# Performance work log

Measured on AMD Instinct MI355X. Metric: run time of the kernel, lower is better.

The kernel has to match this reference:

```python
import jax, jax.numpy as jnp
import numpy as np
import math

D_MODEL = 512
N_HEADS = 8
PATH_LEN = 3
B, L, S = 4, 1024, 1024


def _path_index_structure(L, S, path_length):
    """Precompute the static multi-hop index structure (numpy, trace-time)."""
    i = np.arange(L)[:, None]          # [L,1]
    j = np.arange(S)[None, :]          # [1,S]
    step = (j - i) / path_length       # float
    # Python int() truncates toward zero; i + k*step >= 0 here, so floor == int().
    m1 = np.floor(i + 1 * step).astype(np.int32)  # [L,S] first intermediate point
    m2 = np.floor(i + 2 * step).astype(np.int32)  # [L,S] second intermediate point
    near = np.abs(i - j) <= path_length            # [L,S] bool: direct-score region
    return m1, m2, near


def setup_inputs() -> dict:
    key = jax.random.key(0)
    ks = jax.random.split(key, 7)
    inp = {
        "queries": jax.random.normal(ks[0], (B, L, D_MODEL), dtype=jnp.float32),
        "keys": jax.random.normal(ks[1], (B, S, D_MODEL), dtype=jnp.float32),
        "values": jax.random.normal(ks[2], (B, S, D_MODEL), dtype=jnp.float32),
        # nn.Linear(d_model, d_keys*n_heads, bias=False): stored as [in, out] so y = x @ W
        "W_q": jax.random.normal(ks[3], (D_MODEL, D_MODEL), dtype=jnp.float32) * 0.02,
        "W_k": jax.random.normal(ks[4], (D_MODEL, D_MODEL), dtype=jnp.float32) * 0.02,
        "W_v": jax.random.normal(ks[5], (D_MODEL, D_MODEL), dtype=jnp.float32) * 0.02,
        "W_o": jax.random.normal(ks[6], (D_MODEL, D_MODEL), dtype=jnp.float32) * 0.02,
    }
    return inp


def reference(queries, keys, values, W_q, W_k, W_v, W_o):
    Bv, Lv, _ = queries.shape
    Sv = keys.shape[1]
    H = N_HEADS
    q = (queries @ W_q).reshape(Bv, Lv, H, -1).transpose(0, 2, 1, 3)  # [B,H,L,D]
    k = (keys @ W_k).reshape(Bv, Sv, H, -1).transpose(0, 2, 1, 3)     # [B,H,S,D]
    v = (values @ W_v).reshape(Bv, Sv, H, -1).transpose(0, 2, 1, 3)   # [B,H,S,D]
    D = q.shape[-1]

    scores = jnp.einsum('bhld,bhsd->bhls', q, k) / math.sqrt(D)  # [B,H,L,S]

    # --- path-score modification (vectorized form of the nested loops) ---
    m1, m2, near = _path_index_structure(Lv, Sv, PATH_LEN)
    row = np.arange(Lv)[:, None]
    col = np.arange(Sv)[None, :]
    a = scores[:, :, row, m1]   # scores[:,:,i,m1(i,j)] -> [B,H,L,S]
    b = scores[:, :, m2, col]   # scores[:,:,m2(i,j),j] -> [B,H,L,S]
    # .mean() in the original reduces over BOTH batch and heads to a scalar per (i,j)
    path_mean = jnp.mean(a * b, axis=(0, 1))  # [L,S]
    scores = jnp.where(jnp.asarray(near), scores, path_mean[None, None, :, :])

    attn = jax.nn.softmax(scores, axis=-1)  # dropout p=0 in eval reference
    out = jnp.einsum('bhls,bhsd->blhd', attn, v).reshape(Bv, Lv, H * D)
    out = out @ W_o  # [B,L,d_model]
    return out, attn
```

## Files before the change

kernel.cpp:

```cpp
#include <hip/hip_runtime.h>
#include <math.h>

static constexpr int B_ = 4;
static constexpr int L_ = 1024;
static constexpr int S_ = 1024;
static constexpr int DMODEL = 512;
static constexpr int NH = 8;
static constexpr int DH = 64;
static constexpr int NBH = 32;

typedef __attribute__((ext_vector_type(8))) short s8;
typedef __attribute__((ext_vector_type(4))) float floatx4;

__device__ __forceinline__ short f2bf(float f) {
  unsigned u = __float_as_uint(f);
  return (short)((u + 0x7fffu + ((u >> 16) & 1u)) >> 16);
}
__device__ __forceinline__ float bf2f(short s) {
  return __uint_as_float(((unsigned)(unsigned short)s) << 16);
}

__global__ __launch_bounds__(256)
void cvt_inputs_kernel(const float* __restrict__ q, const float* __restrict__ k,
                       const float* __restrict__ v, short* __restrict__ dst) {
  const int i = blockIdx.x * 256 + threadIdx.x;
  const int arr = i >> 18;
  const int off = (i & 262143) << 3;
  const float* src = (arr == 0) ? q : (arr == 1) ? k : v;
  const float4 f0 = *(const float4*)(src + off);
  const float4 f1 = *(const float4*)(src + off + 4);
  s8 o;
  o[0] = f2bf(f0.x); o[1] = f2bf(f0.y); o[2] = f2bf(f0.z); o[3] = f2bf(f0.w);
  o[4] = f2bf(f1.x); o[5] = f2bf(f1.y); o[6] = f2bf(f1.z); o[7] = f2bf(f1.w);
  *(s8*)(dst + (size_t)arr * 2097152 + off) = o;
}

__global__ __launch_bounds__(256)
void wtrans_kernel(const float* __restrict__ Wq, const float* __restrict__ Wk,
                   const float* __restrict__ Wv, const float* __restrict__ Wo,
                   short* __restrict__ WT) {
  __shared__ float t[32][33];
  const int z = blockIdx.z;
  const float* W = (z == 0) ? Wq : (z == 1) ? Wk : (z == 2) ? Wv : Wo;
  short* dst = WT + (size_t)z * 262144;
  const int k0 = blockIdx.y * 32, n0 = blockIdx.x * 32;
  const int row = threadIdx.x >> 3;
  const int c4 = (threadIdx.x & 7) << 2;
  const float4 f = *(const float4*)(W + (size_t)(k0 + row) * 512 + n0 + c4);
  t[row][c4 + 0] = f.x; t[row][c4 + 1] = f.y; t[row][c4 + 2] = f.z; t[row][c4 + 3] = f.w;
  __syncthreads();
#pragma unroll
  for (int j = 0; j < 4; ++j)
    dst[(size_t)(n0 + row) * 512 + k0 + c4 + j] = f2bf(t[c4 + j][row]);
}

template<int MODE>
__global__ __launch_bounds__(256)
void proj_mfma_kernel(const short* __restrict__ A, const short* __restrict__ WT,
                      void* __restrict__ C, short* __restrict__ C2, int K) {
  const int tid = threadIdx.x;
  const int lane = tid & 63, w = tid >> 6;
  const int wm = w >> 1, wn = w & 1;
  const int m0 = blockIdx.y * 64, n0 = blockIdx.x * 64;
  const int kl = (lane >> 4) << 3;
  const int rA = m0 + wm * 32 + (lane & 15);
  const int rB = n0 + wn * 32 + (lane & 15);
  const short* pA = A + (size_t)rA * K + kl;
  const short* pB = WT + (size_t)rB * K + kl;
  const size_t f16K = (size_t)16 * K;
  floatx4 acc00 = {0,0,0,0}, acc01 = {0,0,0,0}, acc10 = {0,0,0,0}, acc11 = {0,0,0,0};
  for (int k = 0; k < K; k += 32) {
    const s8 a0 = *(const s8*)(pA + k);
    const s8 a1 = *(const s8*)(pA + f16K + k);
    const s8 b0 = *(const s8*)(pB + k);
    const s8 b1 = *(const s8*)(pB + f16K + k);
    acc00 = __builtin_amdgcn_mfma_f32_16x16x32_bf16(a0, b0, acc00, 0, 0, 0);
    acc01 = __builtin_amdgcn_mfma_f32_16x16x32_bf16(a0, b1, acc01, 0, 0, 0);
    acc10 = __builtin_amdgcn_mfma_f32_16x16x32_bf16(a1, b0, acc10, 0, 0, 0);
    acc11 = __builtin_amdgcn_mfma_f32_16x16x32_bf16(a1, b1, acc11, 0, 0, 0);
  }
  const int crow = (lane >> 4) << 2;
  const int ccol = lane & 15;
#pragma unroll
  for (int fm = 0; fm < 2; ++fm)
#pragma unroll
    for (int fn = 0; fn < 2; ++fn) {
      const floatx4 acc = (fm == 0) ? ((fn == 0) ? acc00 : acc01)
                                    : ((fn == 0) ? acc10 : acc11);
      const int col = n0 + wn * 32 + fn * 16 + ccol;
#pragma unroll
      for (int r = 0; r < 4; ++r) {
        const int row = m0 + wm * 32 + fm * 16 + crow + r;
        if (MODE == 0) {
          const int b = row >> 10, l = row & 1023, h = col >> 6, d = col & 63;
          ((short*)C)[((size_t)((b * NH + h) * L_ + l)) * DH + d] = f2bf(acc[r]);
        } else if (MODE == 3) {
          const int b = row >> 10, s = row & 1023, h = col >> 6, d = col & 63;
          const short val = f2bf(acc[r]);
          ((short*)C)[((size_t)((b * NH + h) * DH + d)) * S_ + s] = val;
          C2[((size_t)((b * NH + h) * S_ + s)) * DH + d] = val;
        } else {
          ((float*)C)[(size_t)row * DMODEL + col] = acc[r];
        }
      }
    }
}

__global__ __launch_bounds__(256)
void scores_mfma_kernel(const short* __restrict__ qbf, const short* __restrict__ kbf,
                        float* __restrict__ Sc) {
  const int tid = threadIdx.x;
  const int lane = tid & 63, w = tid >> 6;
  const int wm = w >> 1, wn = w & 1;
  const int m0 = blockIdx.y * 64, n0 = blockIdx.x * 64;
  const int bh = blockIdx.z;
  const int kl = (lane >> 4) << 3;
  const short* pA = qbf + (size_t)bh * L_ * DH + (size_t)(m0 + wm * 32 + (lane & 15)) * DH + kl;
  const short* pB = kbf + (size_t)bh * S_ * DH + (size_t)(n0 + wn * 32 + (lane & 15)) * DH + kl;
  floatx4 acc00 = {0,0,0,0}, acc01 = {0,0,0,0}, acc10 = {0,0,0,0}, acc11 = {0,0,0,0};
#pragma unroll
  for (int k = 0; k < DH; k += 32) {
    const s8 a0 = *(const s8*)(pA + k);
    const s8 a1 = *(const s8*)(pA + 16 * DH + k);
    const s8 b0 = *(const s8*)(pB + k);
    const s8 b1 = *(const s8*)(pB + 16 * DH + k);
    acc00 = __builtin_amdgcn_mfma_f32_16x16x32_bf16(a0, b0, acc00, 0, 0, 0);
    acc01 = __builtin_amdgcn_mfma_f32_16x16x32_bf16(a0, b1, acc01, 0, 0, 0);
    acc10 = __builtin_amdgcn_mfma_f32_16x16x32_bf16(a1, b0, acc10, 0, 0, 0);
    acc11 = __builtin_amdgcn_mfma_f32_16x16x32_bf16(a1, b1, acc11, 0, 0, 0);
  }
  float* Cp = Sc + (size_t)bh * L_ * S_;
  const int crow = (lane >> 4) << 2;
  const int ccol = lane & 15;
#pragma unroll
  for (int fm = 0; fm < 2; ++fm)
#pragma unroll
    for (int fn = 0; fn < 2; ++fn) {
      const floatx4 acc = (fm == 0) ? ((fn == 0) ? acc00 : acc01)
                                    : ((fn == 0) ? acc10 : acc11);
      const int col = n0 + wn * 32 + fn * 16 + ccol;
#pragma unroll
      for (int r = 0; r < 4; ++r) {
        const int row = m0 + wm * 32 + fm * 16 + crow + r;
        Cp[(size_t)row * S_ + col] = acc[r] * 0.125f;
      }
    }
}

__global__ __launch_bounds__(256)
void path_mean_kernel(const float* __restrict__ Sc, float* __restrict__ pm) {
  __shared__ float As[32][36];
  __shared__ float Bs[32][36];
  const int orig = blockIdx.x;
  const int wgid = (orig & 7) * 128 + (orig >> 3);
  const int i0 = (wgid >> 5) << 5;
  const int j0 = (wgid & 31) << 5;
  const int c0 = (2 * i0 + j0) / 3;
  const int c0_al = c0 & ~3;
  const int r0 = (i0 + 2 * j0) / 3;
  const int tid = threadIdx.x;
  const int row_s = tid >> 3;
  const int c4 = tid & 7;
  const int ti = tid >> 3;
  const int tj = tid & 7;
  const int gi = i0 + ti;
  int aoff[4], boff[4];
#pragma unroll
  for (int b = 0; b < 4; ++b) {
    const int gj = j0 + 4 * tj + b;
    const int m1 = (2 * gi + gj) / 3;
    const int m2 = (gi + 2 * gj) / 3;
    aoff[b] = ti * 36 + (m1 - c0_al);
    boff[b] = (m2 - r0) * 36 + (4 * tj + b);
  }
  const int gcA = c0_al + 4 * c4;
  int gcA2 = c0_al + 32; if (gcA2 > 1020) gcA2 = 1020;
  const float* pA  = Sc + (size_t)(i0 + row_s) * S_ + gcA;
  const float* pA2 = Sc + (size_t)(i0 + (tid & 31)) * S_ + gcA2;
  const float* pB  = Sc + (size_t)(r0 + row_s) * S_ + j0 + 4 * c4;
  const float* As0 = &As[0][0];
  const float* Bs0 = &Bs[0][0];
  float acc[4] = {0.f, 0.f, 0.f, 0.f};
  for (int z = 0; z < NBH; ++z) {
    const size_t zo = (size_t)z * (L_ * S_);
    const float4 av = *(const float4*)(pA + zo);
    const float4 bv = *(const float4*)(pB + zo);
    float4 av2;
    if (tid < 32) av2 = *(const float4*)(pA2 + zo);
    __syncthreads();
    *(float4*)&As[row_s][4 * c4] = av;
    if (tid < 32) *(float4*)&As[tid][32] = av2;
    *(float4*)&Bs[row_s][4 * c4] = bv;
    __syncthreads();
#pragma unroll
    for (int b = 0; b < 4; ++b)
      acc[b] = fmaf(As0[aoff[b]], Bs0[boff[b]], acc[b]);
  }
  float4 o = make_float4(acc[0] * (1.f / 32.f), acc[1] * (1.f / 32.f),
                         acc[2] * (1.f / 32.f), acc[3] * (1.f / 32.f));
  *(float4*)&pm[(size_t)gi * S_ + j0 + 4 * tj] = o;
}

__global__ __launch_bounds__(256)
void pm_stats_kernel(const float* __restrict__ pm, short* __restrict__ E,
                     float* __restrict__ pmmax, float* __restrict__ pmsum) {
  const int wid = threadIdx.x >> 6, lane = threadIdx.x & 63;
  const int i = blockIdx.x * 4 + wid;
  const float* row = pm + (size_t)i * S_;
  const int j0 = lane << 4;
  float v[16];
#pragma unroll
  for (int c = 0; c < 4; ++c) {
    const float4 f = *(const float4*)(row + j0 + c * 4);
    v[c * 4 + 0] = f.x; v[c * 4 + 1] = f.y; v[c * 4 + 2] = f.z; v[c * 4 + 3] = f.w;
  }
  float mx = -1e30f;
#pragma unroll
  for (int u = 0; u < 16; ++u) {
    const int d = i - (j0 + u);
    const bool far = (d > 3) || (d < -3);
    if (far) mx = fmaxf(mx, v[u]);
  }
#pragma unroll
  for (int off = 32; off >= 1; off >>= 1) mx = fmaxf(mx, __shfl_xor(mx, off));
  float sum = 0.f;
  short e[16];
#pragma unroll
  for (int u = 0; u < 16; ++u) {
    const int d = i - (j0 + u);
    const bool far = (d > 3) || (d < -3);
    const float ev = far ? __expf(v[u] - mx) : 0.f;
    sum += ev;
    e[u] = f2bf(ev);
  }
#pragma unroll
  for (int off = 32; off >= 1; off >>= 1) sum += __shfl_xor(sum, off);
  s8 o0, o1;
#pragma unroll
  for (int u = 0; u < 8; ++u) { o0[u] = e[u]; o1[u] = e[8 + u]; }
  short* Erow = E + (size_t)i * S_ + j0;
  *(s8*)Erow = o0;
  *(s8*)(Erow + 8) = o1;
  if (lane == 0) { pmmax[i] = mx; pmsum[i] = sum; }
}

__global__ __launch_bounds__(256)
void attn_write_kernel(float* __restrict__ Sc, const short* __restrict__ E,
                       const float* __restrict__ pmmax, const float* __restrict__ pmsum,
                       float* __restrict__ cvec, float* __restrict__ band) {
  const int wid = threadIdx.x >> 6, lane = threadIdx.x & 63;
  const int i = blockIdx.x * 4 + wid;
  const int bh = blockIdx.y;
  float* row = Sc + ((size_t)bh * L_ + i) * S_;

  const int j_u = i - 3 + lane;
  float s_u = -1e30f;
  if (lane < 7 && j_u >= 0 && j_u < S_) s_u = row[j_u];

  float bm = s_u;
#pragma unroll
  for (int off = 32; off >= 1; off >>= 1) bm = fmaxf(bm, __shfl_xor(bm, off));
  const float pmx = pmmax[i];
  const float m = fmaxf(pmx, bm);
  const float bexp = __expf(s_u - m);
  float bsum = bexp;
#pragma unroll
  for (int off = 32; off >= 1; off >>= 1) bsum += __shfl_xor(bsum, off);
  const float cpm = __expf(pmx - m);
  const float inv = 1.f / (bsum + pmsum[i] * cpm);
  const float c = cpm * inv;

  if (lane == 0) cvec[bh * L_ + i] = c;
  if (lane < 8) band[((size_t)(bh * L_ + i)) << 3 | lane] = __expf(s_u - m) * inv;

  const short* Erow = E + (size_t)i * S_;
  const int j0 = lane << 4;
  const s8 e0 = *(const s8*)(Erow + j0);
  const s8 e1 = *(const s8*)(Erow + j0 + 8);
  float outv[16];
#pragma unroll
  for (int u = 0; u < 8; ++u) {
    outv[u]     = bf2f(e0[u]) * c;
    outv[8 + u] = bf2f(e1[u]) * c;
  }
#pragma unroll
  for (int t = 0; t < 16; ++t) {
    const int j = j0 + t;
    const int d = j - i;
    if (d >= -3 && d <= 3)
      outv[t] = __expf(row[j] - m) * inv;
  }
#pragma unroll
  for (int c4 = 0; c4 < 4; ++c4)
    *(float4*)(row + j0 + c4 * 4) =
        make_float4(outv[c4 * 4], outv[c4 * 4 + 1], outv[c4 * 4 + 2], outv[c4 * 4 + 3]);
}

__global__ __launch_bounds__(256)
void ev_kernel(const short* __restrict__ E, const short* __restrict__ vT,
               const short* __restrict__ vS, const float* __restrict__ cvec,
               const float* __restrict__ band, short* __restrict__ out1) {
  const int tid = threadIdx.x;
  const int lane = tid & 63, w = tid >> 6;
  const int wm = w >> 1, wn = w & 1;
  const int m0 = blockIdx.x * 64;
  const int bh = blockIdx.y;
  const int b = bh >> 3, h = bh & 7;
  const int kl = (lane >> 4) << 3;
  const short* pA = E + (size_t)(m0 + wm * 32 + (lane & 15)) * S_ + kl;
  const short* pB = vT + (size_t)bh * DH * S_ + (size_t)(wn * 32 + (lane & 15)) * S_ + kl;
  floatx4 acc00 = {0,0,0,0}, acc01 = {0,0,0,0}, acc10 = {0,0,0,0}, acc11 = {0,0,0,0};
  for (int k = 0; k < S_; k += 32) {
    const s8 a0 = *(const s8*)(pA + k);
    const s8 a1 = *(const s8*)(pA + 16 * S_ + k);
    const s8 b0 = *(const s8*)(pB + k);
    const s8 b1 = *(const s8*)(pB + 16 * S_ + k);
    acc00 = __builtin_amdgcn_mfma_f32_16x16x32_bf16(a0, b0, acc00, 0, 0, 0);
    acc01 = __builtin_amdgcn_mfma_f32_16x16x32_bf16(a0, b1, acc01, 0, 0, 0);
    acc10 = __builtin_amdgcn_mfma_f32_16x16x32_bf16(a1, b0, acc10, 0, 0, 0);
    acc11 = __builtin_amdgcn_mfma_f32_16x16x32_bf16(a1, b1, acc11, 0, 0, 0);
  }
  const int crow = (lane >> 4) << 2;
  const int ccol = lane & 15;
#pragma unroll
  for (int fm = 0; fm < 2; ++fm)
#pragma unroll
    for (int r = 0; r < 4; ++r) {
      const int l = m0 + wm * 32 + fm * 16 + crow + r;
      const float c = cvec[bh * L_ + l];
      const float* bap = band + (((size_t)(bh * L_ + l)) << 3);
      const float4 b0v = *(const float4*)bap;
      const float4 b1v = *(const float4*)(bap + 4);
      const float bav[7] = {b0v.x, b0v.y, b0v.z, b0v.w, b1v.x, b1v.y, b1v.z};
#pragma unroll
      for (int fn = 0; fn < 2; ++fn) {
        const floatx4 acc = (fm == 0) ? ((fn == 0) ? acc00 : acc01)
                                      : ((fn == 0) ? acc10 : acc11);
        const int d = wn * 32 + fn * 16 + ccol;
        float corr = 0.f;
#pragma unroll
        for (int u = 0; u < 7; ++u) {
          int j = l - 3 + u;
          const int jc = j < 0 ? 0 : (j > 1023 ? 1023 : j);
          corr = fmaf(bav[u], bf2f(vS[((size_t)bh * S_ + jc) * DH + d]), corr);
        }
        const float val = fmaf(c, acc[r], corr);
        out1[((size_t)(b * L_ + l)) * DMODEL + h * DH + d] = f2bf(val);
      }
    }
}

extern "C" void kernel_launch(void* const* d_in, const int* in_sizes, int n_in,
                              void* d_out, int out_size, void* d_ws, size_t ws_size,
                              hipStream_t stream) {
  const float* queries = (const float*)d_in[0];
  const float* keys    = (const float*)d_in[1];
  const float* values  = (const float*)d_in[2];
  const float* Wq      = (const float*)d_in[3];
  const float* Wk      = (const float*)d_in[4];
  const float* Wv      = (const float*)d_in[5];
  const float* Wo      = (const float*)d_in[6];

  float* out  = (float*)d_out;
  float* attn = out + (size_t)B_ * L_ * DMODEL;

  char* ws = (char*)d_ws;
  short* xbf  = (short*)(ws);
  short* WT   = (short*)(ws + 12u * 1048576);
  short* qbf  = (short*)(ws + 14u * 1048576);
  short* kbf  = (short*)(ws + 18u * 1048576);
  short* vT   = (short*)(ws + 22u * 1048576);
  short* vS   = (short*)(ws + 26u * 1048576);
  float* pm   = (float*)(ws + 30u * 1048576);
  short* E    = (short*)(ws + 34u * 1048576);
  float* pmmax= (float*)(ws + 36u * 1048576);
  float* pmsum= (float*)(ws + 36u * 1048576 + 4096);
  float* cvec = (float*)(ws + 36u * 1048576 + 65536);
  float* band = (float*)(ws + 37u * 1048576);
  short* out1 = (short*)(ws + 38u * 1048576);

  const dim3 blk(256);

  hipLaunchKernelGGL(cvt_inputs_kernel, dim3(3072), blk, 0, stream,
                     queries, keys, values, xbf);
  hipLaunchKernelGGL(wtrans_kernel, dim3(16, 16, 4), blk, 0, stream,
                     Wq, Wk, Wv, Wo, WT);

  const dim3 gProj(DMODEL / 64, (B_ * L_) / 64);
  hipLaunchKernelGGL((proj_mfma_kernel<0>), gProj, blk, 0, stream,
                     xbf,           WT,          (void*)qbf, (short*)nullptr, DMODEL);
  hipLaunchKernelGGL((proj_mfma_kernel<0>), gProj, blk, 0, stream,
                     xbf + 2097152, WT + 262144, (void*)kbf, (short*)nullptr, DMODEL);
  hipLaunchKernelGGL((proj_mfma_kernel<3>), gProj, blk, 0, stream,
                     xbf + 4194304, WT + 524288, (void*)vT,  vS,              DMODEL);

  const dim3 gSc(S_ / 64, L_ / 64, NBH);
  hipLaunchKernelGGL(scores_mfma_kernel, gSc, blk, 0, stream, qbf, kbf, attn);

  hipLaunchKernelGGL(path_mean_kernel, dim3(1024), blk, 0, stream, attn, pm);

  hipLaunchKernelGGL(pm_stats_kernel, dim3(L_ / 4), blk, 0, stream,
                     pm, E, pmmax, pmsum);

  hipLaunchKernelGGL(attn_write_kernel, dim3(L_ / 4, NBH), blk, 0, stream,
                     attn, E, pmmax, pmsum, cvec, band);

  hipLaunchKernelGGL(ev_kernel, dim3(L_ / 64, NBH), blk, 0, stream,
                     E, vT, vS, cvec, band, out1);

  hipLaunchKernelGGL((proj_mfma_kernel<2>), gProj, blk, 0, stream,
                     out1, WT + 786432, (void*)out, (short*)nullptr, DMODEL);
}
```

Measured before the change: 225.6 us.

## Fuse score computation into path-mean kernel and stop materializing full scores

The separate scores GEMM that wrote the full fp32 [B,H,L,S] score tensor is removed. The path-mean kernel now recomputes the needed 32x32 QK^T tiles per (b,h) with MFMA into LDS and reduces across waves. The attn-write kernel recomputes only the 7 near-diagonal scores as short dot products. In addition, the Q and K projections are batched into one launch over a z-dimension, and ev_kernel stages its band of V rows in LDS. Together these remove a large round trip of the score tensor through global memory, at the cost of redundant MFMA work (two tiles per block per bh) and a serial per-wave loop over heads.

Result: no change. 227.1 us (+0.7%).

```diff
diff --git a/kernel.cpp b/kernel.cpp
--- a/kernel.cpp
+++ b/kernel.cpp
@@ -58,6 +58,9 @@
 __global__ __launch_bounds__(256)
 void proj_mfma_kernel(const short* __restrict__ A, const short* __restrict__ WT,
                       void* __restrict__ C, short* __restrict__ C2, int K) {
+  const int z = blockIdx.z;
+  A  += (size_t)z * 2097152;
+  WT += (size_t)z * 262144;
   const int tid = threadIdx.x;
   const int lane = tid & 63, w = tid >> 6;
   const int wm = w >> 1, wn = w & 1;
@@ -93,7 +96,8 @@
         const int row = m0 + wm * 32 + fm * 16 + crow + r;
         if (MODE == 0) {
           const int b = row >> 10, l = row & 1023, h = col >> 6, d = col & 63;
-          ((short*)C)[((size_t)((b * NH + h) * L_ + l)) * DH + d] = f2bf(acc[r]);
+          ((short*)C)[(size_t)z * 2097152 +
+                      ((size_t)((b * NH + h) * L_ + l)) * DH + d] = f2bf(acc[r]);
         } else if (MODE == 3) {
           const int b = row >> 10, s = row & 1023, h = col >> 6, d = col & 63;
           const short val = f2bf(acc[r]);
@@ -107,98 +111,101 @@
 }
 
 __global__ __launch_bounds__(256)
-void scores_mfma_kernel(const short* __restrict__ qbf, const short* __restrict__ kbf,
-                        float* __restrict__ Sc) {
-  const int tid = threadIdx.x;
-  const int lane = tid & 63, w = tid >> 6;
-  const int wm = w >> 1, wn = w & 1;
-  const int m0 = blockIdx.y * 64, n0 = blockIdx.x * 64;
-  const int bh = blockIdx.z;
-  const int kl = (lane >> 4) << 3;
-  const short* pA = qbf + (size_t)bh * L_ * DH + (size_t)(m0 + wm * 32 + (lane & 15)) * DH + kl;
-  const short* pB = kbf + (size_t)bh * S_ * DH + (size_t)(n0 + wn * 32 + (lane & 15)) * DH + kl;
-  floatx4 acc00 = {0,0,0,0}, acc01 = {0,0,0,0}, acc10 = {0,0,0,0}, acc11 = {0,0,0,0};
-#pragma unroll
-  for (int k = 0; k < DH; k += 32) {
-    const s8 a0 = *(const s8*)(pA + k);
-    const s8 a1 = *(const s8*)(pA + 16 * DH + k);
-    const s8 b0 = *(const s8*)(pB + k);
-    const s8 b1 = *(const s8*)(pB + 16 * DH + k);
-    acc00 = __builtin_amdgcn_mfma_f32_16x16x32_bf16(a0, b0, acc00, 0, 0, 0);
-    acc01 = __builtin_amdgcn_mfma_f32_16x16x32_bf16(a0, b1, acc01, 0, 0, 0);
-    acc10 = __builtin_amdgcn_mfma_f32_16x16x32_bf16(a1, b0, acc10, 0, 0, 0);
-    acc11 = __builtin_amdgcn_mfma_f32_16x16x32_bf16(a1, b1, acc11, 0, 0, 0);
-  }
-  float* Cp = Sc + (size_t)bh * L_ * S_;
-  const int crow = (lane >> 4) << 2;
-  const int ccol = lane & 15;
-#pragma unroll
-  for (int fm = 0; fm < 2; ++fm)
-#pragma unroll
-    for (int fn = 0; fn < 2; ++fn) {
-      const floatx4 acc = (fm == 0) ? ((fn == 0) ? acc00 : acc01)
-                                    : ((fn == 0) ? acc10 : acc11);
-      const int col = n0 + wn * 32 + fn * 16 + ccol;
-#pragma unroll
-      for (int r = 0; r < 4; ++r) {
-        const int row = m0 + wm * 32 + fm * 16 + crow + r;
-        Cp[(size_t)row * S_ + col] = acc[r] * 0.125f;
-      }
-    }
-}
-
-__global__ __launch_bounds__(256)
-void path_mean_kernel(const float* __restrict__ Sc, float* __restrict__ pm) {
-  __shared__ float As[32][36];
-  __shared__ float Bs[32][36];
+void pm_fused_kernel(const short* __restrict__ qbf, const short* __restrict__ kbf,
+                     float* __restrict__ pm) {
+  __shared__ __align__(16) float SA[4][32][33];
+  __shared__ __align__(16) float SB[4][32][33];
+
   const int orig = blockIdx.x;
   const int wgid = (orig & 7) * 128 + (orig >> 3);
   const int i0 = (wgid >> 5) << 5;
   const int j0 = (wgid & 31) << 5;
   const int c0 = (2 * i0 + j0) / 3;
-  const int c0_al = c0 & ~3;
   const int r0 = (i0 + 2 * j0) / 3;
+
   const int tid = threadIdx.x;
-  const int row_s = tid >> 3;
-  const int c4 = tid & 7;
-  const int ti = tid >> 3;
-  const int tj = tid & 7;
-  const int gi = i0 + ti;
-  int aoff[4], boff[4];
-#pragma unroll
-  for (int b = 0; b < 4; ++b) {
-    const int gj = j0 + 4 * tj + b;
+  const int lane = tid & 63, w = tid >> 6;
+  const int frow = lane & 15;
+  const int kl = (lane >> 4) << 3;
+  const int ti = lane & 31;
+  const int tjb = (lane >> 5) << 4;
+
+  int aoff[16], boff[16];
+#pragma unroll
+  for (int u = 0; u < 16; ++u) {
+    const int gi = i0 + ti, gj = j0 + tjb + u;
     const int m1 = (2 * gi + gj) / 3;
     const int m2 = (gi + 2 * gj) / 3;
-    aoff[b] = ti * 36 + (m1 - c0_al);
-    boff[b] = (m2 - r0) * 36 + (4 * tj + b);
-  }
-  const int gcA = c0_al + 4 * c4;
-  int gcA2 = c0_al + 32; if (gcA2 > 1020) gcA2 = 1020;
-  const float* pA  = Sc + (size_t)(i0 + row_s) * S_ + gcA;
-  const float* pA2 = Sc + (size_t)(i0 + (tid & 31)) * S_ + gcA2;
-  const float* pB  = Sc + (size_t)(r0 + row_s) * S_ + j0 + 4 * c4;
-  const float* As0 = &As[0][0];
-  const float* Bs0 = &Bs[0][0];
-  float acc[4] = {0.f, 0.f, 0.f, 0.f};
-  for (int z = 0; z < NBH; ++z) {
-    const size_t zo = (size_t)z * (L_ * S_);
-    const float4 av = *(const float4*)(pA + zo);
-    const float4 bv = *(const float4*)(pB + zo);
-    float4 av2;
-    if (tid < 32) av2 = *(const float4*)(pA2 + zo);
-    __syncthreads();
-    *(float4*)&As[row_s][4 * c4] = av;
-    if (tid < 32) *(float4*)&As[tid][32] = av2;
-    *(float4*)&Bs[row_s][4 * c4] = bv;
-    __syncthreads();
-#pragma unroll
-    for (int b = 0; b < 4; ++b)
-      acc[b] = fmaf(As0[aoff[b]], Bs0[boff[b]], acc[b]);
-  }
-  float4 o = make_float4(acc[0] * (1.f / 32.f), acc[1] * (1.f / 32.f),
-                         acc[2] * (1.f / 32.f), acc[3] * (1.f / 32.f));
-  *(float4*)&pm[(size_t)gi * S_ + j0 + 4 * tj] = o;
+    aoff[u] = ti * 33 + (m1 - c0);
+    boff[u] = (m2 - r0) * 33 + (tjb + u);
+  }
+  float acc[16];
+#pragma unroll
+  for (int u = 0; u < 16; ++u) acc[u] = 0.f;
+
+  float* SAw = &SA[w][0][0];
+  float* SBw = &SB[w][0][0];
+  const int crow = (lane >> 4) << 2;
+  const int ccol = lane & 15;
+
+  for (int bh = w; bh < NBH; bh += 4) {
+    const short* Qb = qbf + (size_t)bh * L_ * DH;
+    const short* Kb = kbf + (size_t)bh * S_ * DH;
+#pragma unroll
+    for (int t = 0; t < 2; ++t) {
+      const int rb = t ? r0 : i0;
+      const int cb = t ? j0 : c0;
+      const short* pQ = Qb + (size_t)(rb + frow) * DH + kl;
+      const short* pK = Kb + (size_t)(cb + frow) * DH + kl;
+      floatx4 a00 = {0,0,0,0}, a01 = {0,0,0,0}, a10 = {0,0,0,0}, a11 = {0,0,0,0};
+#pragma unroll
+      for (int ks = 0; ks < DH; ks += 32) {
+        const s8 qa = *(const s8*)(pQ + ks);
+        const s8 qb2 = *(const s8*)(pQ + 16 * DH + ks);
+        const s8 ka = *(const s8*)(pK + ks);
+        const s8 kb2 = *(const s8*)(pK + 16 * DH + ks);
+        a00 = __builtin_amdgcn_mfma_f32_16x16x32_bf16(qa,  ka,  a00, 0, 0, 0);
+        a01 = __builtin_amdgcn_mfma_f32_16x16x32_bf16(qa,  kb2, a01, 0, 0, 0);
+        a10 = __builtin_amdgcn_mfma_f32_16x16x32_bf16(qb2, ka,  a10, 0, 0, 0);
+        a11 = __builtin_amdgcn_mfma_f32_16x16x32_bf16(qb2, kb2, a11, 0, 0, 0);
+      }
+      float* dst = t ? SBw : SAw;
+#pragma unroll
+      for (int fm = 0; fm < 2; ++fm)
+#pragma unroll
+        for (int fn = 0; fn < 2; ++fn) {
+          const floatx4 a = (fm == 0) ? ((fn == 0) ? a00 : a01)
+                                      : ((fn == 0) ? a10 : a11);
+#pragma unroll
+          for (int r = 0; r < 4; ++r)
+            dst[(fm * 16 + crow + r) * 33 + fn * 16 + ccol] = a[r] * 0.125f;
+        }
+    }
+#pragma unroll
+    for (int u = 0; u < 16; ++u)
+      acc[u] = fmaf(SAw[aoff[u]], SBw[boff[u]], acc[u]);
+  }
+
+  __syncthreads();
+  float* P = &SA[0][0][0];
+#pragma unroll
+  for (int u4 = 0; u4 < 4; ++u4) {
+    float4 v4 = make_float4(acc[u4 * 4], acc[u4 * 4 + 1],
+                            acc[u4 * 4 + 2], acc[u4 * 4 + 3]);
+    *(float4*)&P[w * 1152 + ti * 36 + tjb + u4 * 4] = v4;
+  }
+  __syncthreads();
+  const int ti2 = tid >> 3;
+  const int tj2 = (tid & 7) << 2;
+  float4 ssum = make_float4(0.f, 0.f, 0.f, 0.f);
+#pragma unroll
+  for (int w2 = 0; w2 < 4; ++w2) {
+    const float4 v = *(const float4*)&P[w2 * 1152 + ti2 * 36 + tj2];
+    ssum.x += v.x; ssum.y += v.y; ssum.z += v.z; ssum.w += v.w;
+  }
+  ssum.x *= (1.f / 32.f); ssum.y *= (1.f / 32.f);
+  ssum.z *= (1.f / 32.f); ssum.w *= (1.f / 32.f);
+  *(float4*)&pm[(size_t)(i0 + ti2) * S_ + j0 + tj2] = ssum;
 }
 
 __global__ __launch_bounds__(256)
@@ -245,17 +252,29 @@
 }
 
 __global__ __launch_bounds__(256)
-void attn_write_kernel(float* __restrict__ Sc, const short* __restrict__ E,
+void attn_write_kernel(float* __restrict__ attnOut, const short* __restrict__ E,
                        const float* __restrict__ pmmax, const float* __restrict__ pmsum,
+                       const short* __restrict__ qbf, const short* __restrict__ kbf,
                        float* __restrict__ cvec, float* __restrict__ band) {
   const int wid = threadIdx.x >> 6, lane = threadIdx.x & 63;
   const int i = blockIdx.x * 4 + wid;
   const int bh = blockIdx.y;
-  float* row = Sc + ((size_t)bh * L_ + i) * S_;
 
   const int j_u = i - 3 + lane;
   float s_u = -1e30f;
-  if (lane < 7 && j_u >= 0 && j_u < S_) s_u = row[j_u];
+  if (lane < 7 && j_u >= 0 && j_u < S_) {
+    const short* qr = qbf + ((size_t)bh * L_ + i) * DH;
+    const short* kr = kbf + ((size_t)bh * S_ + j_u) * DH;
+    float d0 = 0.f;
+#pragma unroll
+    for (int c = 0; c < 8; ++c) {
+      const s8 qv = *(const s8*)(qr + c * 8);
+      const s8 kv = *(const s8*)(kr + c * 8);
+#pragma unroll
+      for (int e = 0; e < 8; ++e) d0 = fmaf(bf2f(qv[e]), bf2f(kv[e]), d0);
+    }
+    s_u = d0 * 0.125f;
+  }
 
   float bm = s_u;
 #pragma unroll
@@ -271,8 +290,13 @@
   const float c = cpm * inv;
 
   if (lane == 0) cvec[bh * L_ + i] = c;
-  if (lane < 8) band[((size_t)(bh * L_ + i)) << 3 | lane] = __expf(s_u - m) * inv;
-
+  if (lane < 8) band[((size_t)(bh * L_ + i)) << 3 | lane] = bexp * inv;
+
+  float bb[7];
+#pragma unroll
+  for (int u = 0; u < 7; ++u) bb[u] = __shfl(bexp, u) * inv;
+
+  float* row = attnOut + ((size_t)bh * L_ + i) * S_;
   const short* Erow = E + (size_t)i * S_;
   const int j0 = lane << 4;
   const s8 e0 = *(const s8*)(Erow + j0);
@@ -285,10 +309,8 @@
   }
 #pragma unroll
   for (int t = 0; t < 16; ++t) {
-    const int j = j0 + t;
-    const int d = j - i;
-    if (d >= -3 && d <= 3)
-      outv[t] = __expf(row[j] - m) * inv;
+    const int d = (j0 + t) - i;
+    if (d >= -3 && d <= 3) outv[t] = bb[d + 3];
   }
 #pragma unroll
   for (int c4 = 0; c4 < 4; ++c4)
@@ -300,12 +322,21 @@
 void ev_kernel(const short* __restrict__ E, const short* __restrict__ vT,
                const short* __restrict__ vS, const float* __restrict__ cvec,
                const float* __restrict__ band, short* __restrict__ out1) {
+  __shared__ short Vb[70 * 64];
   const int tid = threadIdx.x;
-  const int lane = tid & 63, w = tid >> 6;
-  const int wm = w >> 1, wn = w & 1;
   const int m0 = blockIdx.x * 64;
   const int bh = blockIdx.y;
   const int b = bh >> 3, h = bh & 7;
+
+  for (int idx = tid; idx < 560; idx += 256) {
+    const int rr = idx >> 3, c8 = (idx & 7) << 3;
+    int j = m0 - 3 + rr; j = j < 0 ? 0 : (j > 1023 ? 1023 : j);
+    *(s8*)&Vb[rr * 64 + c8] = *(const s8*)(vS + ((size_t)bh * S_ + j) * DH + c8);
+  }
+  __syncthreads();
+
+  const int lane = tid & 63, w = tid >> 6;
+  const int wm = w >> 1, wn = w & 1;
   const int kl = (lane >> 4) << 3;
   const short* pA = E + (size_t)(m0 + wm * 32 + (lane & 15)) * S_ + kl;
   const short* pB = vT + (size_t)bh * DH * S_ + (size_t)(wn * 32 + (lane & 15)) * S_ + kl;
@@ -327,6 +358,7 @@
 #pragma unroll
     for (int r = 0; r < 4; ++r) {
       const int l = m0 + wm * 32 + fm * 16 + crow + r;
+      const int lrel = (l - m0);
       const float c = cvec[bh * L_ + l];
       const float* bap = band + (((size_t)(bh * L_ + l)) << 3);
       const float4 b0v = *(const float4*)bap;
@@ -339,11 +371,8 @@
         const int d = wn * 32 + fn * 16 + ccol;
         float corr = 0.f;
 #pragma unroll
-        for (int u = 0; u < 7; ++u) {
-          int j = l - 3 + u;
-          const int jc = j < 0 ? 0 : (j > 1023 ? 1023 : j);
-          corr = fmaf(bav[u], bf2f(vS[((size_t)bh * S_ + jc) * DH + d]), corr);
-        }
+        for (int u = 0; u < 7; ++u)
+          corr = fmaf(bav[u], bf2f(Vb[(lrel + u) * 64 + d]), corr);
         const float val = fmaf(c, acc[r], corr);
         out1[((size_t)(b * L_ + l)) * DMODEL + h * DH + d] = f2bf(val);
       }
@@ -386,24 +415,20 @@
   hipLaunchKernelGGL(wtrans_kernel, dim3(16, 16, 4), blk, 0, stream,
                      Wq, Wk, Wv, Wo, WT);
 
+  const dim3 gProjQK(DMODEL / 64, (B_ * L_) / 64, 2);
+  hipLaunchKernelGGL((proj_mfma_kernel<0>), gProjQK, blk, 0, stream,
+                     xbf, WT, (void*)qbf, (short*)nullptr, DMODEL);
   const dim3 gProj(DMODEL / 64, (B_ * L_) / 64);
-  hipLaunchKernelGGL((proj_mfma_kernel<0>), gProj, blk, 0, stream,
-                     xbf,           WT,          (void*)qbf, (short*)nullptr, DMODEL);
-  hipLaunchKernelGGL((proj_mfma_kernel<0>), gProj, blk, 0, stream,
-                     xbf + 2097152, WT + 262144, (void*)kbf, (short*)nullptr, DMODEL);
   hipLaunchKernelGGL((proj_mfma_kernel<3>), gProj, blk, 0, stream,
-                     xbf + 4194304, WT + 524288, (void*)vT,  vS,              DMODEL);
-
-  const dim3 gSc(S_ / 64, L_ / 64, NBH);
-  hipLaunchKernelGGL(scores_mfma_kernel, gSc, blk, 0, stream, qbf, kbf, attn);
-
-  hipLaunchKernelGGL(path_mean_kernel, dim3(1024), blk, 0, stream, attn, pm);
+                     xbf + 4194304, WT + 524288, (void*)vT, vS, DMODEL);
+
+  hipLaunchKernelGGL(pm_fused_kernel, dim3(1024), blk, 0, stream, qbf, kbf, pm);
 
   hipLaunchKernelGGL(pm_stats_kernel, dim3(L_ / 4), blk, 0, stream,
                      pm, E, pmmax, pmsum);
 
   hipLaunchKernelGGL(attn_write_kernel, dim3(L_ / 4, NBH), blk, 0, stream,
-                     attn, E, pmmax, pmsum, cvec, band);
+                     attn, E, pmmax, pmsum, qbf, kbf, cvec, band);
 
   hipLaunchKernelGGL(ev_kernel, dim3(L_ / 64, NBH), blk, 0, stream,
                      E, vT, vS, cvec, band, out1);
```

## Store scores in bf16 scratch, fuse attn write into EV kernel, merge QKV projections

Applied to the files above, without the earlier changes.

Scores are written as bf16 to a workspace buffer instead of fp32 into the attn output, with the diagonal band saved separately in fp32. The path-mean kernel reads the bf16 scores, and the separate attn_write pass is folded into the E·V MFMA loop, which writes final attention rows while streaming E. The three QKV projections become one launch, and V band rows are staged in shared memory. The goal is to cut the fp32 score write/read traffic and launch count; path_mean now uses bf16-rounded scores, which lowers its precision.

After: 202.2 us (median of 2 runs). 10.4% less time.

```diff
diff --git a/kernel.cpp b/kernel.cpp
--- a/kernel.cpp
+++ b/kernel.cpp
@@ -22,8 +22,14 @@
 
 __global__ __launch_bounds__(256)
 void cvt_inputs_kernel(const float* __restrict__ q, const float* __restrict__ k,
-                       const float* __restrict__ v, short* __restrict__ dst) {
+                       const float* __restrict__ v, short* __restrict__ dst,
+                       float* __restrict__ bandS) {
   const int i = blockIdx.x * 256 + threadIdx.x;
+  if (i < 32768) {
+    const float4 m4 = make_float4(-1e30f, -1e30f, -1e30f, -1e30f);
+    *(float4*)(bandS + ((size_t)i << 3)) = m4;
+    *(float4*)(bandS + ((size_t)i << 3) + 4) = m4;
+  }
   const int arr = i >> 18;
   const int off = (i & 262143) << 3;
   const float* src = (arr == 0) ? q : (arr == 1) ? k : v;
@@ -54,19 +60,21 @@
     dst[(size_t)(n0 + row) * 512 + k0 + c4 + j] = f2bf(t[c4 + j][row]);
 }
 
-template<int MODE>
-__global__ __launch_bounds__(256)
-void proj_mfma_kernel(const short* __restrict__ A, const short* __restrict__ WT,
-                      void* __restrict__ C, short* __restrict__ C2, int K) {
+__global__ __launch_bounds__(256)
+void proj_qkv_kernel(const short* __restrict__ xbf, const short* __restrict__ WTall,
+                     short* __restrict__ qk, short* __restrict__ vT,
+                     short* __restrict__ vS) {
+  const int z = blockIdx.z;
+  const short* A = xbf + (size_t)z * 2097152;
+  const short* WT = WTall + (size_t)z * 262144;
+  const int K = DMODEL;
   const int tid = threadIdx.x;
   const int lane = tid & 63, w = tid >> 6;
   const int wm = w >> 1, wn = w & 1;
   const int m0 = blockIdx.y * 64, n0 = blockIdx.x * 64;
   const int kl = (lane >> 4) << 3;
-  const int rA = m0 + wm * 32 + (lane & 15);
-  const int rB = n0 + wn * 32 + (lane & 15);
-  const short* pA = A + (size_t)rA * K + kl;
-  const short* pB = WT + (size_t)rB * K + kl;
+  const short* pA = A + (size_t)(m0 + wm * 32 + (lane & 15)) * K + kl;
+  const short* pB = WT + (size_t)(n0 + wn * 32 + (lane & 15)) * K + kl;
   const size_t f16K = (size_t)16 * K;
   floatx4 acc00 = {0,0,0,0}, acc01 = {0,0,0,0}, acc10 = {0,0,0,0}, acc11 = {0,0,0,0};
   for (int k = 0; k < K; k += 32) {
@@ -91,24 +99,21 @@
 #pragma unroll
       for (int r = 0; r < 4; ++r) {
         const int row = m0 + wm * 32 + fm * 16 + crow + r;
-        if (MODE == 0) {
-          const int b = row >> 10, l = row & 1023, h = col >> 6, d = col & 63;
-          ((short*)C)[((size_t)((b * NH + h) * L_ + l)) * DH + d] = f2bf(acc[r]);
-        } else if (MODE == 3) {
-          const int b = row >> 10, s = row & 1023, h = col >> 6, d = col & 63;
-          const short val = f2bf(acc[r]);
-          ((short*)C)[((size_t)((b * NH + h) * DH + d)) * S_ + s] = val;
-          C2[((size_t)((b * NH + h) * S_ + s)) * DH + d] = val;
+        const int b = row >> 10, l = row & 1023, h = col >> 6, d = col & 63;
+        const short val = f2bf(acc[r]);
+        if (z < 2) {
+          qk[(size_t)z * 2097152 + ((size_t)((b * NH + h) * L_ + l)) * DH + d] = val;
         } else {
-          ((float*)C)[(size_t)row * DMODEL + col] = acc[r];
+          vT[((size_t)((b * NH + h) * DH + d)) * S_ + l] = val;
+          vS[((size_t)((b * NH + h) * S_ + l)) * DH + d] = val;
         }
       }
     }
 }
 
 __global__ __launch_bounds__(256)
-void scores_mfma_kernel(const short* __restrict__ qbf, const short* __restrict__ kbf,
-                        float* __restrict__ Sc) {
+void scores_bf16_kernel(const short* __restrict__ qbf, const short* __restrict__ kbf,
+                        short* __restrict__ Sbf, float* __restrict__ bandS) {
   const int tid = threadIdx.x;
   const int lane = tid & 63, w = tid >> 6;
   const int wm = w >> 1, wn = w & 1;
@@ -129,7 +134,7 @@
     acc10 = __builtin_amdgcn_mfma_f32_16x16x32_bf16(a1, b0, acc10, 0, 0, 0);
     acc11 = __builtin_amdgcn_mfma_f32_16x16x32_bf16(a1, b1, acc11, 0, 0, 0);
   }
-  float* Cp = Sc + (size_t)bh * L_ * S_;
+  short* Sp = Sbf + ((size_t)bh << 20);
   const int crow = (lane >> 4) << 2;
   const int ccol = lane & 15;
 #pragma unroll
@@ -142,25 +147,27 @@
 #pragma unroll
       for (int r = 0; r < 4; ++r) {
         const int row = m0 + wm * 32 + fm * 16 + crow + r;
-        Cp[(size_t)row * S_ + col] = acc[r] * 0.125f;
-      }
-    }
-}
-
-__global__ __launch_bounds__(256)
-void path_mean_kernel(const float* __restrict__ Sc, float* __restrict__ pm) {
-  __shared__ float As[32][36];
+        const float sc = acc[r] * 0.125f;
+        Sp[(size_t)row * S_ + col] = f2bf(sc);
+        const int dd = col - row;
+        if (dd >= -3 && dd <= 3)
+          bandS[(((size_t)bh << 10) + row) * 8 + dd + 3] = sc;
+      }
+    }
+}
+
+__global__ __launch_bounds__(256)
+void path_mean_kernel(const short* __restrict__ Sbf, float* __restrict__ pm) {
+  __shared__ float As[32][44];
   __shared__ float Bs[32][36];
   const int orig = blockIdx.x;
   const int wgid = (orig & 7) * 128 + (orig >> 3);
   const int i0 = (wgid >> 5) << 5;
   const int j0 = (wgid & 31) << 5;
   const int c0 = (2 * i0 + j0) / 3;
-  const int c0_al = c0 & ~3;
+  const int c0a = c0 & ~7;
   const int r0 = (i0 + 2 * j0) / 3;
   const int tid = threadIdx.x;
-  const int row_s = tid >> 3;
-  const int c4 = tid & 7;
   const int ti = tid >> 3;
   const int tj = tid & 7;
   const int gi = i0 + ti;
@@ -170,27 +177,50 @@
     const int gj = j0 + 4 * tj + b;
     const int m1 = (2 * gi + gj) / 3;
     const int m2 = (gi + 2 * gj) / 3;
-    aoff[b] = ti * 36 + (m1 - c0_al);
+    aoff[b] = ti * 44 + (m1 - c0a);
     boff[b] = (m2 - r0) * 36 + (4 * tj + b);
   }
-  const int gcA = c0_al + 4 * c4;
-  int gcA2 = c0_al + 32; if (gcA2 > 1020) gcA2 = 1020;
-  const float* pA  = Sc + (size_t)(i0 + row_s) * S_ + gcA;
-  const float* pA2 = Sc + (size_t)(i0 + (tid & 31)) * S_ + gcA2;
-  const float* pB  = Sc + (size_t)(r0 + row_s) * S_ + j0 + 4 * c4;
+  const int uA = tid;
+  const int uB2 = tid + 256;
+  int arow = 0, ac = 0, brow = 0, bc = 0, brow2 = 0, bc2 = 0;
+  bool isA = uA < 160;
+  if (isA) { arow = uA / 5; ac = uA - arow * 5; }
+  else { const int v = uA - 160; brow = v >> 2; bc = v & 3; }
+  const bool hasU2 = tid < 32;
+  { const int v = uB2 - 160; brow2 = v >> 2; bc2 = v & 3; }
+  int gcA = c0a + (ac << 3); if (gcA > 1016) gcA = 1016;
+  const short* pA = Sbf + (size_t)(i0 + arow) * S_ + gcA;
+  const short* pB = Sbf + (size_t)(r0 + brow) * S_ + j0 + (bc << 3);
+  const short* pB2 = Sbf + (size_t)(r0 + brow2) * S_ + j0 + (bc2 << 3);
+
   const float* As0 = &As[0][0];
   const float* Bs0 = &Bs[0][0];
   float acc[4] = {0.f, 0.f, 0.f, 0.f};
   for (int z = 0; z < NBH; ++z) {
-    const size_t zo = (size_t)z * (L_ * S_);
-    const float4 av = *(const float4*)(pA + zo);
-    const float4 bv = *(const float4*)(pB + zo);
-    float4 av2;
-    if (tid < 32) av2 = *(const float4*)(pA2 + zo);
+    const size_t zo = (size_t)z << 20;
+    const s8 v1 = isA ? *(const s8*)(pA + zo) : *(const s8*)(pB + zo);
+    s8 v2;
+    if (hasU2) v2 = *(const s8*)(pB2 + zo);
     __syncthreads();
-    *(float4*)&As[row_s][4 * c4] = av;
-    if (tid < 32) *(float4*)&As[tid][32] = av2;
-    *(float4*)&Bs[row_s][4 * c4] = bv;
+    {
+      float4 lo, hi;
+      lo.x = bf2f(v1[0]); lo.y = bf2f(v1[1]); lo.z = bf2f(v1[2]); lo.w = bf2f(v1[3]);
+      hi.x = bf2f(v1[4]); hi.y = bf2f(v1[5]); hi.z = bf2f(v1[6]); hi.w = bf2f(v1[7]);
+      if (isA) {
+        *(float4*)&As[arow][ac << 3] = lo;
+        *(float4*)&As[arow][(ac << 3) + 4] = hi;
+      } else {
+        *(float4*)&Bs[brow][bc << 3] = lo;
+        *(float4*)&Bs[brow][(bc << 3) + 4] = hi;
+      }
+      if (hasU2) {
+        float4 lo2, hi2;
+        lo2.x = bf2f(v2[0]); lo2.y = bf2f(v2[1]); lo2.z = bf2f(v2[2]); lo2.w = bf2f(v2[3]);
+        hi2.x = bf2f(v2[4]); hi2.y = bf2f(v2[5]); hi2.z = bf2f(v2[6]); hi2.w = bf2f(v2[7]);
+        *(float4*)&Bs[brow2][bc2 << 3] = lo2;
+        *(float4*)&Bs[brow2][(bc2 << 3) + 4] = hi2;
+      }
+    }
     __syncthreads();
 #pragma unroll
     for (int b = 0; b < 4; ++b)
@@ -245,70 +275,59 @@
 }
 
 __global__ __launch_bounds__(256)
-void attn_write_kernel(float* __restrict__ Sc, const short* __restrict__ E,
-                       const float* __restrict__ pmmax, const float* __restrict__ pmsum,
-                       float* __restrict__ cvec, float* __restrict__ band) {
-  const int wid = threadIdx.x >> 6, lane = threadIdx.x & 63;
-  const int i = blockIdx.x * 4 + wid;
-  const int bh = blockIdx.y;
-  float* row = Sc + ((size_t)bh * L_ + i) * S_;
-
-  const int j_u = i - 3 + lane;
-  float s_u = -1e30f;
-  if (lane < 7 && j_u >= 0 && j_u < S_) s_u = row[j_u];
-
-  float bm = s_u;
-#pragma unroll
-  for (int off = 32; off >= 1; off >>= 1) bm = fmaxf(bm, __shfl_xor(bm, off));
-  const float pmx = pmmax[i];
-  const float m = fmaxf(pmx, bm);
-  const float bexp = __expf(s_u - m);
-  float bsum = bexp;
-#pragma unroll
-  for (int off = 32; off >= 1; off >>= 1) bsum += __shfl_xor(bsum, off);
-  const float cpm = __expf(pmx - m);
-  const float inv = 1.f / (bsum + pmsum[i] * cpm);
-  const float c = cpm * inv;
-
-  if (lane == 0) cvec[bh * L_ + i] = c;
-  if (lane < 8) band[((size_t)(bh * L_ + i)) << 3 | lane] = __expf(s_u - m) * inv;
-
-  const short* Erow = E + (size_t)i * S_;
-  const int j0 = lane << 4;
-  const s8 e0 = *(const s8*)(Erow + j0);
-  const s8 e1 = *(const s8*)(Erow + j0 + 8);
-  float outv[16];
-#pragma unroll
-  for (int u = 0; u < 8; ++u) {
-    outv[u]     = bf2f(e0[u]) * c;
-    outv[8 + u] = bf2f(e1[u]) * c;
-  }
-#pragma unroll
-  for (int t = 0; t < 16; ++t) {
-    const int j = j0 + t;
-    const int d = j - i;
-    if (d >= -3 && d <= 3)
-      outv[t] = __expf(row[j] - m) * inv;
-  }
-#pragma unroll
-  for (int c4 = 0; c4 < 4; ++c4)
-    *(float4*)(row + j0 + c4 * 4) =
-        make_float4(outv[c4 * 4], outv[c4 * 4 + 1], outv[c4 * 4 + 2], outv[c4 * 4 + 3]);
-}
-
-__global__ __launch_bounds__(256)
-void ev_kernel(const short* __restrict__ E, const short* __restrict__ vT,
-               const short* __restrict__ vS, const float* __restrict__ cvec,
-               const float* __restrict__ band, short* __restrict__ out1) {
+void ev_fused_kernel(const short* __restrict__ E, const short* __restrict__ vT,
+                     const short* __restrict__ vS, const float* __restrict__ bandS,
+                     const float* __restrict__ pmmax, const float* __restrict__ pmsum,
+                     float* __restrict__ attn, short* __restrict__ out1) {
+  __shared__ float cL[64];
+  __shared__ float bL[64][8];
+  __shared__ short Vb[70 * 64];
   const int tid = threadIdx.x;
-  const int lane = tid & 63, w = tid >> 6;
-  const int wm = w >> 1, wn = w & 1;
   const int m0 = blockIdx.x * 64;
   const int bh = blockIdx.y;
   const int b = bh >> 3, h = bh & 7;
+
+  for (int idx = tid; idx < 560; idx += 256) {
+    const int rr = idx >> 3, c8 = (idx & 7) << 3;
+    int j = m0 - 3 + rr; j = j < 0 ? 0 : (j > 1023 ? 1023 : j);
+    *(s8*)&Vb[rr * 64 + c8] = *(const s8*)(vS + ((size_t)bh * S_ + j) * DH + c8);
+  }
+
+  {
+    const int r = tid >> 2, p = tid & 3;
+    const int l = m0 + r;
+    const float pmx = pmmax[l], psum = pmsum[l];
+    const float* bs = bandS + (((size_t)bh << 10) + l) * 8;
+    const float sa = bs[p], sb2 = bs[p + 4];
+    float mx = fmaxf(sa, sb2);
+    mx = fmaxf(mx, __shfl_xor(mx, 1));
+    mx = fmaxf(mx, __shfl_xor(mx, 2));
+    const float m = fmaxf(mx, pmx);
+    const float ea = __expf(sa - m), eb = __expf(sb2 - m);
+    float bsum = ea + eb;
+    bsum += __shfl_xor(bsum, 1);
+    bsum += __shfl_xor(bsum, 2);
+    const float cpm = __expf(pmx - m);
+    const float inv = 1.f / (bsum + psum * cpm);
+    if (p == 0) cL[r] = cpm * inv;
+    bL[r][p] = ea * inv;
+    bL[r][p + 4] = eb * inv;
+  }
+  __syncthreads();
+
+  const int lane = tid & 63, w = tid >> 6;
+  const int wm = w >> 1, wn = w & 1;
+  const int frow = lane & 15;
   const int kl = (lane >> 4) << 3;
-  const short* pA = E + (size_t)(m0 + wm * 32 + (lane & 15)) * S_ + kl;
-  const short* pB = vT + (size_t)bh * DH * S_ + (size_t)(wn * 32 + (lane & 15)) * S_ + kl;
+  const int ra0 = m0 + wm * 32 + frow;
+  const int lr0 = wm * 32 + frow;
+  const int lr1 = lr0 + 16;
+  const short* pA = E + (size_t)ra0 * S_ + kl;
+  const short* pB = vT + (size_t)bh * DH * S_ + (size_t)(wn * 32 + frow) * S_ + kl;
+  const float c0v = cL[lr0];
+  const float c1v = cL[lr1];
+  float* arow0 = attn + ((size_t)bh * L_ + ra0) * S_;
+  float* arow1 = arow0 + (size_t)16 * S_;
   floatx4 acc00 = {0,0,0,0}, acc01 = {0,0,0,0}, acc10 = {0,0,0,0}, acc11 = {0,0,0,0};
   for (int k = 0; k < S_; k += 32) {
     const s8 a0 = *(const s8*)(pA + k);
@@ -319,18 +338,49 @@
     acc01 = __builtin_amdgcn_mfma_f32_16x16x32_bf16(a0, b1, acc01, 0, 0, 0);
     acc10 = __builtin_amdgcn_mfma_f32_16x16x32_bf16(a1, b0, acc10, 0, 0, 0);
     acc11 = __builtin_amdgcn_mfma_f32_16x16x32_bf16(a1, b1, acc11, 0, 0, 0);
-  }
+    const int jw = k + kl;
+    if (wn == 0) {
+      float att[8];
+#pragma unroll
+      for (int e = 0; e < 8; ++e) att[e] = bf2f(a0[e]) * c0v;
+      const int rel = ra0 - jw;
+      if ((unsigned)(rel + 3) <= 13u) {
+#pragma unroll
+        for (int e = 0; e < 8; ++e) {
+          const int d = e - rel;
+          if ((unsigned)(d + 3) <= 6u) att[e] = bL[lr0][d + 3];
+        }
+      }
+      *(float4*)(arow0 + jw) = make_float4(att[0], att[1], att[2], att[3]);
+      *(float4*)(arow0 + jw + 4) = make_float4(att[4], att[5], att[6], att[7]);
+    } else {
+      float att[8];
+#pragma unroll
+      for (int e = 0; e < 8; ++e) att[e] = bf2f(a1[e]) * c1v;
+      const int rel = ra0 + 16 - jw;
+      if ((unsigned)(rel + 3) <= 13u) {
+#pragma unroll
+        for (int e = 0; e < 8; ++e) {
+          const int d = e - rel;
+          if ((unsigned)(d + 3) <= 6u) att[e] = bL[lr1][d + 3];
+        }
+      }
+      *(float4*)(arow1 + jw) = make_float4(att[0], att[1], att[2], att[3]);
+      *(float4*)(arow1 + jw + 4) = make_float4(att[4], att[5], att[6], att[7]);
+    }
+  }
+
   const int crow = (lane >> 4) << 2;
   const int ccol = lane & 15;
 #pragma unroll
   for (int fm = 0; fm < 2; ++fm)
 #pragma unroll
     for (int r = 0; r < 4; ++r) {
-      const int l = m0 + wm * 32 + fm * 16 + crow + r;
-      const float c = cvec[bh * L_ + l];
-      const float* bap = band + (((size_t)(bh * L_ + l)) << 3);
-      const float4 b0v = *(const float4*)bap;
-      const float4 b1v = *(const float4*)(bap + 4);
+      const int lrel = wm * 32 + fm * 16 + crow + r;
+      const int l = m0 + lrel;
+      const float cc = cL[lrel];
+      const float4 b0v = *(const float4*)&bL[lrel][0];
+      const float4 b1v = *(const float4*)&bL[lrel][4];
       const float bav[7] = {b0v.x, b0v.y, b0v.z, b0v.w, b1v.x, b1v.y, b1v.z};
 #pragma unroll
       for (int fn = 0; fn < 2; ++fn) {
@@ -339,13 +389,50 @@
         const int d = wn * 32 + fn * 16 + ccol;
         float corr = 0.f;
 #pragma unroll
-        for (int u = 0; u < 7; ++u) {
-          int j = l - 3 + u;
-          const int jc = j < 0 ? 0 : (j > 1023 ? 1023 : j);
-          corr = fmaf(bav[u], bf2f(vS[((size_t)bh * S_ + jc) * DH + d]), corr);
-        }
-        const float val = fmaf(c, acc[r], corr);
+        for (int u = 0; u < 7; ++u)
+          corr = fmaf(bav[u], bf2f(Vb[(lrel + u) * 64 + d]), corr);
+        const float val = fmaf(cc, acc[r], corr);
         out1[((size_t)(b * L_ + l)) * DMODEL + h * DH + d] = f2bf(val);
+      }
+    }
+}
+
+__global__ __launch_bounds__(256)
+void proj_out_kernel(const short* __restrict__ A, const short* __restrict__ WT,
+                     float* __restrict__ C) {
+  const int K = DMODEL;
+  const int tid = threadIdx.x;
+  const int lane = tid & 63, w = tid >> 6;
+  const int wm = w >> 1, wn = w & 1;
+  const int m0 = blockIdx.y * 64, n0 = blockIdx.x * 64;
+  const int kl = (lane >> 4) << 3;
+  const short* pA = A + (size_t)(m0 + wm * 32 + (lane & 15)) * K + kl;
+  const short* pB = WT + (size_t)(n0 + wn * 32 + (lane & 15)) * K + kl;
+  const size_t f16K = (size_t)16 * K;
+  floatx4 acc00 = {0,0,0,0}, acc01 = {0,0,0,0}, acc10 = {0,0,0,0}, acc11 = {0,0,0,0};
+  for (int k = 0; k < K; k += 32) {
+    const s8 a0 = *(const s8*)(pA + k);
+    const s8 a1 = *(const s8*)(pA + f16K + k);
+    const s8 b0 = *(const s8*)(pB + k);
+    const s8 b1 = *(const s8*)(pB + f16K + k);
+    acc00 = __builtin_amdgcn_mfma_f32_16x16x32_bf16(a0, b0, acc00, 0, 0, 0);
+    acc01 = __builtin_amdgcn_mfma_f32_16x16x32_bf16(a0, b1, acc01, 0, 0, 0);
+    acc10 = __builtin_amdgcn_mfma_f32_16x16x32_bf16(a1, b0, acc10, 0, 0, 0);
+    acc11 = __builtin_amdgcn_mfma_f32_16x16x32_bf16(a1, b1, acc11, 0, 0, 0);
+  }
+  const int crow = (lane >> 4) << 2;
+  const int ccol = lane & 15;
+#pragma unroll
+  for (int fm = 0; fm < 2; ++fm)
+#pragma unroll
+    for (int fn = 0; fn < 2; ++fn) {
+      const floatx4 acc = (fm == 0) ? ((fn == 0) ? acc00 : acc01)
+                                    : ((fn == 0) ? acc10 : acc11);
+      const int col = n0 + wn * 32 + fn * 16 + ccol;
+#pragma unroll
+      for (int r = 0; r < 4; ++r) {
+        const int row = m0 + wm * 32 + fm * 16 + crow + r;
+        C[(size_t)row * DMODEL + col] = acc[r];
       }
     }
 }
@@ -365,49 +452,40 @@
   float* attn = out + (size_t)B_ * L_ * DMODEL;
 
   char* ws = (char*)d_ws;
-  short* xbf  = (short*)(ws);
-  short* WT   = (short*)(ws + 12u * 1048576);
-  short* qbf  = (short*)(ws + 14u * 1048576);
-  short* kbf  = (short*)(ws + 18u * 1048576);
-  short* vT   = (short*)(ws + 22u * 1048576);
-  short* vS   = (short*)(ws + 26u * 1048576);
-  float* pm   = (float*)(ws + 30u * 1048576);
-  short* E    = (short*)(ws + 34u * 1048576);
-  float* pmmax= (float*)(ws + 36u * 1048576);
-  float* pmsum= (float*)(ws + 36u * 1048576 + 4096);
-  float* cvec = (float*)(ws + 36u * 1048576 + 65536);
-  float* band = (float*)(ws + 37u * 1048576);
-  short* out1 = (short*)(ws + 38u * 1048576);
+  short* xbf   = (short*)(ws);
+  short* WT    = (short*)(ws + 12u * 1048576);
+  short* qkbf  = (short*)(ws + 14u * 1048576);
+  short* vT    = (short*)(ws + 22u * 1048576);
+  short* vS    = (short*)(ws + 26u * 1048576);
+  float* pm    = (float*)(ws + 30u * 1048576);
+  short* E     = (short*)(ws + 34u * 1048576);
+  float* pmmax = (float*)(ws + 36u * 1048576);
+  float* pmsum = (float*)(ws + 36u * 1048576 + 4096);
+  float* bandS = (float*)(ws + 37u * 1048576);
+  short* out1  = (short*)(ws + 38u * 1048576);
+  short* Sbf   = (short*)(ws + 42u * 1048576);
 
   const dim3 blk(256);
 
   hipLaunchKernelGGL(cvt_inputs_kernel, dim3(3072), blk, 0, stream,
-                     queries, keys, values, xbf);
+                     queries, keys, values, xbf, bandS);
   hipLaunchKernelGGL(wtrans_kernel, dim3(16, 16, 4), blk, 0, stream,
                      Wq, Wk, Wv, Wo, WT);
 
-  const dim3 gProj(DMODEL / 64, (B_ * L_) / 64);
-  hipLaunchKernelGGL((proj_mfma_kernel<0>), gProj, blk, 0, stream,
-                     xbf,           WT,          (void*)qbf, (short*)nullptr, DMODEL);
-  hipLaunchKernelGGL((proj_mfma_kernel<0>), gProj, blk, 0, stream,
-                     xbf + 2097152, WT + 262144, (void*)kbf, (short*)nullptr, DMODEL);
-  hipLaunchKernelGGL((proj_mfma_kernel<3>), gProj, blk, 0, stream,
-                     xbf + 4194304, WT + 524288, (void*)vT,  vS,              DMODEL);
-
-  const dim3 gSc(S_ / 64, L_ / 64, NBH);
-  hipLaunchKernelGGL(scores_mfma_kernel, gSc, blk, 0, stream, qbf, kbf, attn);
-
-  hipLaunchKernelGGL(path_mean_kernel, dim3(1024), blk, 0, stream, attn, pm);
+  hipLaunchKernelGGL(proj_qkv_kernel, dim3(DMODEL / 64, (B_ * L_) / 64, 3),
+                     blk, 0, stream, xbf, WT, qkbf, vT, vS);
+
+  hipLaunchKernelGGL(scores_bf16_kernel, dim3(S_ / 64, L_ / 64, NBH), blk, 0, stream,
+                     qkbf, qkbf + 2097152, Sbf, bandS);
+
+  hipLaunchKernelGGL(path_mean_kernel, dim3(1024), blk, 0, stream, Sbf, pm);
 
   hipLaunchKernelGGL(pm_stats_kernel, dim3(L_ / 4), blk, 0, stream,
                      pm, E, pmmax, pmsum);
 
-  hipLaunchKernelGGL(attn_write_kernel, dim3(L_ / 4, NBH), blk, 0, stream,
-                     attn, E, pmmax, pmsum, cvec, band);
-
-  hipLaunchKernelGGL(ev_kernel, dim3(L_ / 64, NBH), blk, 0, stream,
-                     E, vT, vS, cvec, band, out1);
-
-  hipLaunchKernelGGL((proj_mfma_kernel<2>), gProj, blk, 0, stream,
-                     out1, WT + 786432, (void*)out, (short*)nullptr, DMODEL);
-}
+  hipLaunchKernelGGL(ev_fused_kernel, dim3(L_ / 64, NBH), blk, 0, stream,
+                     E, vT, vS, bandS, pmmax, pmsum, attn, out1);
+
+  hipLaunchKernelGGL(proj_out_kernel, dim3(DMODEL / 64, (B_ * L_) / 64), blk, 0, stream,
+                     out1, WT + 786432, out);
+}
```
